# Kernel optimization log

Measured on AMD Instinct MI355X. Metric: run time of the kernel, lower is better.

Reference implementation:

```python
import jax, jax.numpy as jnp
import numpy as np

WAYS, SHOTS = 32, 64
N = WAYS * SHOTS
XDIM, CIN = 84, 3
FLAT = 10 * 19 * 19  # 3610 after conv/pool stack
ZDIM = 2 * 32 * 4    # 256

def _conv2d(x, w, b):
    y = jax.lax.conv_general_dilated(x, w, (1, 1), 'VALID',
        dimension_numbers=('NCHW', 'OIHW', 'NCHW'))
    return y + b[None, :, None, None]

def _maxpool2(x):
    return jax.lax.reduce_window(x, -jnp.inf, jax.lax.max,
        (1, 1, 2, 2), (1, 1, 2, 2), 'VALID')

def setup_inputs() -> dict:
    key = jax.random.key(0)
    ks = jax.random.split(key, 32)
    rn = lambda k, shape, s=0.05: jax.random.normal(k, shape, jnp.float32) * s
    labels = jax.random.randint(ks[0], (N,), 0, WAYS)
    y = jax.nn.one_hot(labels, WAYS, dtype=jnp.float32)
    z = lambda n: jnp.zeros((n,), jnp.float32)
    return {
        'x': jax.random.normal(ks[1], (N, CIN, XDIM, XDIM), jnp.float32),
        'y': y,
        'conv1_w': rn(ks[2], (10, CIN, 3, 3)), 'conv1_b': z(10),
        'conv2_w': rn(ks[3], (10, 10, 3, 3)), 'conv2_b': z(10),
        'enc_w': rn(ks[4], (FLAT, 64)), 'enc_b': z(64),
        't1_w': rn(ks[5], (3, 4), 0.2), 't1_b': z(4),
        'te2_w1': rn(ks[6], (256, 128)), 'te2_b1': z(128),
        'te2_w2': rn(ks[7], (128, 32)), 'te2_b2': z(32),
        't2_w': rn(ks[8], (3, 4), 0.2), 't2_b': z(4),
        'om_mu_w': rn(ks[9], (256, 1)), 'om_mu_b': z(1),
        'om_sd_w': rn(ks[10], (256, 1)), 'om_sd_b': z(1),
        'ga_w': rn(ks[11], (128, 64)), 'ga_b': z(64),
        'ga_mu_w': rn(ks[12], (64, 5)), 'ga_mu_b': z(5),
        'ga_sd_w': rn(ks[13], (64, 5)), 'ga_sd_b': z(5),
        'ze_w': rn(ks[14], (128, 64)), 'ze_b': z(64),
        'ze_mu_w': rn(ks[15], (64, ZDIM)), 'ze_mu_b': z(ZDIM),
        'ze_sd_w': rn(ks[16], (64, ZDIM)), 'ze_sd_b': z(ZDIM),
        'do_sample': 0,
    }

def _kl_std_normal(mu, sigma):
    # KL(N(mu, sigma) || N(0, 1)), summed
    return jnp.sum(-jnp.log(sigma) + 0.5 * (sigma * sigma + mu * mu) - 0.5)

def _forward(x, y, conv1_w, conv1_b, conv2_w, conv2_b, enc_w, enc_b,
             t1_w, t1_b, te2_w1, te2_b1, te2_w2, te2_b2, t2_w, t2_b,
             om_mu_w, om_mu_b, om_sd_w, om_sd_b,
             ga_w, ga_b, ga_mu_w, ga_mu_b, ga_sd_w, ga_sd_b,
             ze_w, ze_b, ze_mu_w, ze_mu_b, ze_sd_w, ze_sd_b):
    relu = jax.nn.relu
    # class encoder: conv-relu-pool x2 + flatten + linear -> [N, 64]
    h = _maxpool2(relu(_conv2d(x, conv1_w, conv1_b)))
    h = _maxpool2(relu(_conv2d(h, conv2_w, conv2_b)))
    h = h.reshape(h.shape[0], -1) @ enc_w + enc_b  # [N, 64]
    # statistics_pooling_1: per-class masked var/mean/cardinality (vectorized over classes)
    y_sum = jnp.sum(y, axis=1)           # [N]
    y_arg = jnp.argmax(y, axis=1)        # [N]
    cls_mask = ((y_arg[None, :] == jnp.arange(WAYS)[:, None]) &
                (y_sum[None, :] > 0)).astype(jnp.float32)  # [W, N]
    xm = h[None, :, :] * cls_mask[:, :, None]              # [W, N, 64]
    mean = jnp.mean(xm, axis=1)                            # [W, 64]
    var = jnp.var(xm, axis=1, ddof=1)                      # unbiased, matches torch.var_mean
    card = (jnp.sum(y[None, :, :] * cls_mask[:, :, None], axis=(1, 2)) - 1.0) / (SHOTS - 1.0)  # [W]
    cs = jnp.stack([mean, var, jnp.broadcast_to(card[:, None], (WAYS, 64))], axis=2)  # [W, 64, 3]
    cs = relu(cs @ t1_w + t1_b).reshape(WAYS, -1)          # [W, 256]
    # statistics_pooling_2
    ts = relu(cs @ te2_w1 + te2_b1) @ te2_w2 + te2_b2      # [W, 32]
    t = jnp.stack([jnp.mean(ts, axis=0), jnp.var(ts, axis=0, ddof=1),
                   jnp.broadcast_to(jnp.sum(card), (32,))], axis=1)  # [32, 3]
    t = relu(t @ t2_w + t2_b).reshape(1, -1)               # [1, 128]
    # omega (use_s=True: heads applied to class_summary directly)
    mu_o = relu(cs @ om_mu_w + om_mu_b)[:, 0]              # [W]
    sd_o = jax.nn.softplus(relu(cs @ om_sd_w + om_sd_b)[:, 0])
    # gamma
    eg = relu(t @ ga_w + ga_b)                             # [1, 64]
    mu_g = relu(eg @ ga_mu_w + ga_mu_b)[0]                 # [5]
    sd_g = jax.nn.softplus(relu(eg @ ga_sd_w + ga_sd_b)[0])
    # zeta
    ez = relu(t @ ze_w + ze_b)                             # [1, 64]
    mu_z = relu(ez @ ze_mu_w + ze_mu_b)[0]                 # [256]
    sd_z = jax.nn.softplus(relu(ez @ ze_sd_w + ze_sd_b)[0])
    kl = _kl_std_normal(mu_o, sd_o) + _kl_std_normal(mu_g, sd_g) + _kl_std_normal(mu_z, sd_z)
    # deterministic path (do_sample=False -> distribution means); concat for a single output
    return jnp.concatenate([mu_o, mu_g, mu_z, kl[None]])   # [W + 5 + 256 + 1]

def reference(x, y, conv1_w, conv1_b, conv2_w, conv2_b, enc_w, enc_b,
              t1_w, t1_b, te2_w1, te2_b1, te2_w2, te2_b2, t2_w, t2_b,
              om_mu_w, om_mu_b, om_sd_w, om_sd_b,
              ga_w, ga_b, ga_mu_w, ga_mu_b, ga_sd_w, ga_sd_b,
              ze_w, ze_b, ze_mu_w, ze_mu_b, ze_sd_w, ze_sd_b, do_sample):
    return _forward(x, y, conv1_w, conv1_b, conv2_w, conv2_b, enc_w, enc_b,
                    t1_w, t1_b, te2_w1, te2_b1, te2_w2, te2_b2, t2_w, t2_b,
                    om_mu_w, om_mu_b, om_sd_w, om_sd_b,
                    ga_w, ga_b, ga_mu_w, ga_mu_b, ga_sd_w, ga_sd_b,
                    ze_w, ze_b, ze_mu_w, ze_mu_b, ze_sd_w, ze_sd_b)
```

## Files before the change

kernel.cpp:

```cpp
#include <hip/hip_runtime.h>
#include <math.h>

#define WAYS 32
#define NTOT 2048
#define XD 84
#define FLAT 3610
#define KSPLIT 16
#define KCHUNK 226

__device__ __forceinline__ float softplus_f(float x) {
    return (x > 20.f) ? x : log1pf(expf(x));
}
__device__ __forceinline__ float kl_f(float mu, float sd) {
    return -logf(sd) + 0.5f * (sd * sd + mu * mu) - 0.5f;
}

struct Out10 { float v[10]; };

__global__ __launch_bounds__(256, 4) void k_conv(
        const float* __restrict__ x,
        const float* __restrict__ w1, const float* __restrict__ b1,
        const float* __restrict__ w2, const float* __restrict__ b2,
        float* __restrict__ p2) {
    __shared__ __align__(16) float u_s[3 * 22 * 84];
    __shared__ __align__(16) float w1t[27 * 12];
    __shared__ __align__(16) float w2t[90 * 16];

    const int tid  = threadIdx.x;
    const int img  = blockIdx.x & 2047;
    const int band = blockIdx.x >> 11;
    const int r0   = band * 4;
    const int nr   = (band < 4) ? 4 : 3;
    const int nq   = 2 * nr + 2;
    const int xr0  = 16 * band;
    const int nxr  = 2 * nq + 2;

    {
        const float* xg = x + (size_t)img * (3 * XD * XD);
        const int nv = (nxr * 84) >> 2;
        #pragma unroll
        for (int c = 0; c < 3; c++) {
            const float4* src = (const float4*)(xg + c * (XD * XD) + xr0 * 84);
            float4* dst = (float4*)(u_s + c * (22 * 84));
            for (int i = tid; i < nv; i += 256) dst[i] = src[i];
        }
    }
    for (int i = tid; i < 270; i += 256) {
        int oc = i / 27, r = i - oc * 27;
        w1t[r * 12 + oc] = w1[i];
    }
    for (int i = tid; i < 900; i += 256) {
        int oc = i / 90, r = i - oc * 90;
        int h = oc / 5, o = oc - h * 5;
        w2t[r * 16 + h * 8 + o] = w2[i];
    }
    float b1r[10];
    #pragma unroll
    for (int o = 0; o < 10; o++) b1r[o] = b1[o];
    __syncthreads();

    const int n1 = nq * 40;

    auto conv1_item = [&](int q, int p) -> Out10 {
        float acc[10][4];
        #pragma unroll
        for (int o = 0; o < 10; o++)
            #pragma unroll
            for (int j = 0; j < 4; j++) acc[o][j] = 0.f;
        #pragma unroll 1
        for (int c = 0; c < 3; c++) {
            float xp[4][4];
            #pragma unroll
            for (int rr = 0; rr < 4; rr++) {
                const float2* row =
                    (const float2*)&u_s[c * (22 * 84) + (2 * q + rr) * 84 + 2 * p];
                float2 lo = row[0], hi = row[1];
                xp[rr][0] = lo.x; xp[rr][1] = lo.y;
                xp[rr][2] = hi.x; xp[rr][3] = hi.y;
            }
            #pragma unroll
            for (int ky = 0; ky < 3; ky++) {
                #pragma unroll
                for (int kx = 0; kx < 3; kx++) {
                    const float* wr = &w1t[(c * 9 + ky * 3 + kx) * 12];
                    float4 wA = *(const float4*)(wr);
                    float4 wB = *(const float4*)(wr + 4);
                    float2 wC = *(const float2*)(wr + 8);
                    float wv[10] = {wA.x, wA.y, wA.z, wA.w,
                                    wB.x, wB.y, wB.z, wB.w,
                                    wC.x, wC.y};
                    #pragma unroll
                    for (int o = 0; o < 10; o++) {
                        float w = wv[o];
                        acc[o][0] = fmaf(xp[ky][kx],         w, acc[o][0]);
                        acc[o][1] = fmaf(xp[ky][kx + 1],     w, acc[o][1]);
                        acc[o][2] = fmaf(xp[ky + 1][kx],     w, acc[o][2]);
                        acc[o][3] = fmaf(xp[ky + 1][kx + 1], w, acc[o][3]);
                    }
                }
            }
        }
        Out10 r;
        #pragma unroll
        for (int o = 0; o < 10; o++) {
            float m = fmaxf(fmaxf(acc[o][0], acc[o][1]), fmaxf(acc[o][2], acc[o][3]));
            r.v[o] = fmaxf(m + b1r[o], 0.f);
        }
        return r;
    };

    Out10 A, B;
    {
        int q = tid / 40, p = tid - q * 40;
        A = conv1_item(q, p);
    }
    asm volatile("" ::: "memory");
    const int itB = tid + 256;
    const bool hasB = (itB < n1);
    if (hasB) {
        int q = itB / 40, p = itB - q * 40;
        B = conv1_item(q, p);
    }
    __syncthreads();

    {
        #pragma unroll
        for (int o = 0; o < 10; o++) u_s[o * 400 + tid] = A.v[o];
        if (hasB) {
            #pragma unroll
            for (int o = 0; o < 10; o++) u_s[o * 400 + itB] = B.v[o];
        }
    }
    __syncthreads();

    {
        const int npos = nr * 19;
        if (tid < 152) {
            int half = (tid >= 76) ? 1 : 0;
            int pos  = tid - 76 * half;
            if (pos < npos) {
                int pr = pos / 19;
                int pc = pos - pr * 19;
                float acc[5][4];
                #pragma unroll
                for (int o = 0; o < 5; o++)
                    #pragma unroll
                    for (int j = 0; j < 4; j++) acc[o][j] = 0.f;
                #pragma unroll 1
                for (int ic = 0; ic < 10; ic++) {
                    float xp[4][4];
                    #pragma unroll
                    for (int rr = 0; rr < 4; rr++) {
                        const float2* row =
                            (const float2*)&u_s[ic * 400 + (2 * pr + rr) * 40 + 2 * pc];
                        float2 lo = row[0], hi = row[1];
                        xp[rr][0] = lo.x; xp[rr][1] = lo.y;
                        xp[rr][2] = hi.x; xp[rr][3] = hi.y;
                    }
                    #pragma unroll
                    for (int ky = 0; ky < 3; ky++) {
                        #pragma unroll
                        for (int kx = 0; kx < 3; kx++) {
                            const float* wr = &w2t[(ic * 9 + ky * 3 + kx) * 16 + half * 8];
                            float4 wA = *(const float4*)(wr);
                            float w4 = wr[4];
                            float wv[5] = {wA.x, wA.y, wA.z, wA.w, w4};
                            #pragma unroll
                            for (int o = 0; o < 5; o++) {
                                float w = wv[o];
                                acc[o][0] = fmaf(xp[ky][kx],         w, acc[o][0]);
                                acc[o][1] = fmaf(xp[ky][kx + 1],     w, acc[o][1]);
                                acc[o][2] = fmaf(xp[ky + 1][kx],     w, acc[o][2]);
                                acc[o][3] = fmaf(xp[ky + 1][kx + 1], w, acc[o][3]);
                            }
                        }
                    }
                }
                float* outp = p2 + (size_t)img * FLAT;
                #pragma unroll
                for (int o = 0; o < 5; o++) {
                    int oc = half * 5 + o;
                    float m = fmaxf(fmaxf(acc[o][0], acc[o][1]), fmaxf(acc[o][2], acc[o][3]));
                    outp[oc * 361 + (r0 + pr) * 19 + pc] = fmaxf(m + b2[oc], 0.f);
                }
            }
        }
    }
}

__global__ void k_label(const float* __restrict__ y, int* __restrict__ label) {
    int n = blockIdx.x * 256 + threadIdx.x;
    if (n >= NTOT) return;
    const float* yr = y + n * WAYS;
    float best = yr[0]; int bi = 0;
    for (int k = 1; k < WAYS; k++) {
        float v = yr[k];
        if (v > best) { best = v; bi = k; }
    }
    label[n] = bi;
}

__global__ __launch_bounds__(256, 2) void k_enc(
        const float* __restrict__ A, const float* __restrict__ W,
        float* __restrict__ H) {
    __shared__ float a_s[32 * 66];
    __shared__ float w_s[32 * 64];
    int mb = blockIdx.x >> 4;
    int ks = blockIdx.x & 15;
    int row0 = mb * 64;
    int kbeg = ks * KCHUNK;
    int kend = min(kbeg + KCHUNK, FLAT);
    int tid = threadIdx.x;
    int tr = tid & 15, tc = tid >> 4;
    float acc[4][4] = {};

    for (int k0 = kbeg; k0 < kend; k0 += 32) {
        {
            int kk = tid & 31;
            int r  = tid >> 5;
            int gk = k0 + kk;
            #pragma unroll
            for (int i = 0; i < 8; i++) {
                int rr = r + i * 8;
                float v = (gk < kend) ? A[(size_t)(row0 + rr) * FLAT + gk] : 0.f;
                a_s[kk * 66 + rr] = v;
            }
            int c  = tid & 63;
            int kw = tid >> 6;
            #pragma unroll
            for (int i = 0; i < 8; i++) {
                int kk2 = kw + i * 4;
                int gk2 = k0 + kk2;
                float v = (gk2 < kend) ? W[(size_t)gk2 * 64 + c] : 0.f;
                w_s[kk2 * 64 + c] = v;
            }
        }
        __syncthreads();
        #pragma unroll 8
        for (int k = 0; k < 32; k++) {
            float av[4], wv[4];
            #pragma unroll
            for (int i = 0; i < 4; i++) av[i] = a_s[k * 66 + tr * 4 + i];
            #pragma unroll
            for (int j = 0; j < 4; j++) wv[j] = w_s[k * 64 + tc * 4 + j];
            #pragma unroll
            for (int i = 0; i < 4; i++)
                #pragma unroll
                for (int j = 0; j < 4; j++)
                    acc[i][j] = fmaf(av[i], wv[j], acc[i][j]);
        }
        __syncthreads();
    }
    #pragma unroll
    for (int i = 0; i < 4; i++)
        #pragma unroll
        for (int j = 0; j < 4; j++)
            atomicAdd(&H[(size_t)(row0 + tr * 4 + i) * 64 + tc * 4 + j], acc[i][j]);
}

__global__ __launch_bounds__(1024) void k_stats(
        const float* __restrict__ H, const float* __restrict__ encb,
        const int* __restrict__ label,
        const float* __restrict__ t1w, const float* __restrict__ t1b,
        float* __restrict__ cs, float* __restrict__ card) {
    __shared__ int   lbl_s[NTOT];
    __shared__ float rs[16][64], rs2[16][64];
    __shared__ int rc[16];
    int w = blockIdx.x;
    int tid = threadIdx.x;
    for (int i = tid; i < NTOT; i += 1024) lbl_s[i] = label[i];
    __syncthreads();
    int c = tid & 63, g = tid >> 6;
    float eb = encb[c];
    float s = 0.f, s2 = 0.f; int cnt = 0;
    #pragma unroll 4
    for (int n = g; n < NTOT; n += 16) {
        bool m = (lbl_s[n] == w);
        float hv = H[n * 64 + c] + eb;
        float hm = m ? hv : 0.f;
        s += hm; s2 += hm * hm; cnt += m ? 1 : 0;
    }
    rs[g][c] = s; rs2[g][c] = s2;
    if (c == 0) rc[g] = cnt;
    __syncthreads();
    if (g == 0) {
        float S = 0.f, S2 = 0.f; int CNT = 0;
        #pragma unroll
        for (int gg = 0; gg < 16; gg++) {
            S += rs[gg][c]; S2 += rs2[gg][c]; CNT += rc[gg];
        }
        float mean = S / 2048.f;
        float var  = (S2 - S * S / 2048.f) / 2047.f;
        float cd   = ((float)CNT - 1.f) / 63.f;
        #pragma unroll
        for (int j = 0; j < 4; j++)
            cs[w * 256 + c * 4 + j] =
                fmaxf(mean * t1w[j] + var * t1w[4 + j] + cd * t1w[8 + j] + t1b[j], 0.f);
        if (c == 0) card[w] = cd;
    }
}

__global__ __launch_bounds__(256) void k_head(
        const float* __restrict__ cs_g, const float* __restrict__ card,
        const float* __restrict__ te2w1, const float* __restrict__ te2b1,
        const float* __restrict__ te2w2, const float* __restrict__ te2b2,
        const float* __restrict__ t2w, const float* __restrict__ t2b,
        const float* __restrict__ omw, const float* __restrict__ omb,
        const float* __restrict__ osw, const float* __restrict__ osb,
        const float* __restrict__ gaw, const float* __restrict__ gab,
        const float* __restrict__ gmw, const float* __restrict__ gmb,
        const float* __restrict__ gsw, const float* __restrict__ gsb,
        const float* __restrict__ zew, const float* __restrict__ zeb,
        const float* __restrict__ zmw, const float* __restrict__ zmb,
        const float* __restrict__ zsw, const float* __restrict__ zsb,
        float* __restrict__ out) {
    __shared__ __align__(16) float cst[256 * 36];
    __shared__ __align__(16) float a1t[128 * 36];
    __shared__ float ts[32 * 32];
    __shared__ float tv[128];
    __shared__ float eg_s[64], ez_s[64];
    __shared__ float red[256];
    __shared__ float redb[512];
    int tid = threadIdx.x;

    for (int i = tid; i < 32 * 256; i += 256) {
        int w = i >> 8, k = i & 255;
        cst[k * 36 + w] = cs_g[i];
    }
    __syncthreads();

    {
        int wg = tid >> 5, jg = tid & 31;
        int w0 = wg * 4, j0 = jg * 4;
        float acc[4][4] = {};
        for (int k = 0; k < 256; k++) {
            float4 cv4 = *(const float4*)&cst[k * 36 + w0];
            float4 wv4 = *(const float4*)&te2w1[k * 128 + j0];
            float cva[4] = {cv4.x, cv4.y, cv4.z, cv4.w};
            float wva[4] = {wv4.x, wv4.y, wv4.z, wv4.w};
            #pragma unroll
            for (int i = 0; i < 4; i++)
                #pragma unroll
                for (int j = 0; j < 4; j++)
                    acc[i][j] = fmaf(cva[i], wva[j], acc[i][j]);
        }
        #pragma unroll
        for (int jj = 0; jj < 4; jj++) {
            float b = te2b1[j0 + jj];
            #pragma unroll
            for (int i = 0; i < 4; i++)
                a1t[(j0 + jj) * 36 + w0 + i] = fmaxf(acc[i][jj] + b, 0.f);
        }
    }
    __syncthreads();

    {
        int wg = tid >> 4, jg = tid & 15;
        int w0 = wg * 2, j0 = jg * 2;
        float acc[2][2] = {};
        for (int k = 0; k < 128; k++) {
            float2 a2 = *(const float2*)&a1t[k * 36 + w0];
            float2 b2v = *(const float2*)&te2w2[k * 32 + j0];
            acc[0][0] = fmaf(a2.x, b2v.x, acc[0][0]);
            acc[0][1] = fmaf(a2.x, b2v.y, acc[0][1]);
            acc[1][0] = fmaf(a2.y, b2v.x, acc[1][0]);
            acc[1][1] = fmaf(a2.y, b2v.y, acc[1][1]);
        }
        #pragma unroll
        for (int i = 0; i < 2; i++)
            #pragma unroll
            for (int j = 0; j < 2; j++)
                ts[(w0 + i) * 32 + (j0 + j)] = acc[i][j] + te2b2[j0 + j];
    }

    {
        int w = tid & 31, part = tid >> 5;
        int k0 = part * 32;
        float am = 0.f, as = 0.f;
        #pragma unroll 4
        for (int k = k0; k < k0 + 32; k++) {
            float cv = cst[k * 36 + w];
            am = fmaf(cv, omw[k], am);
            as = fmaf(cv, osw[k], as);
        }
        redb[part * 32 + w] = am;
        redb[256 + part * 32 + w] = as;
    }
    __syncthreads();

    float muo = 0.f, sdo = 1.f;
    if (tid < 32) {
        float am = 0.f, as = 0.f;
        #pragma unroll
        for (int p = 0; p < 8; p++) {
            am += redb[p * 32 + tid];
            as += redb[256 + p * 32 + tid];
        }
        muo = fmaxf(am + omb[0], 0.f);
        sdo = softplus_f(fmaxf(as + osb[0], 0.f));
        out[tid] = muo;
    } else if (tid < 64) {
        int t_ = tid - 32;
        float csum = 0.f;
        for (int w2 = 0; w2 < 32; w2++) csum += card[w2];
        float s = 0.f, s2 = 0.f;
        for (int w2 = 0; w2 < 32; w2++) { float v = ts[w2 * 32 + t_]; s += v; s2 += v * v; }
        float m  = s / 32.f;
        float vv = (s2 - s * s / 32.f) / 31.f;
        #pragma unroll
        for (int j = 0; j < 4; j++)
            tv[t_ * 4 + j] = fmaxf(m * t2w[j] + vv * t2w[4 + j] + csum * t2w[8 + j] + t2b[j], 0.f);
    }
    __syncthreads();

    {
        int j = tid & 63, part = tid >> 6;
        int k0 = part * 32;
        float ag = 0.f, az = 0.f;
        #pragma unroll 4
        for (int k = k0; k < k0 + 32; k++) {
            float t = tv[k];
            ag = fmaf(t, gaw[k * 64 + j], ag);
            az = fmaf(t, zew[k * 64 + j], az);
        }
        redb[part * 64 + j] = ag;
        redb[256 + part * 64 + j] = az;
    }
    __syncthreads();
    if (tid < 64) {
        float ag = gab[tid], az = zeb[tid];
        #pragma unroll
        for (int p = 0; p < 4; p++) {
            ag += redb[p * 64 + tid];
            az += redb[256 + p * 64 + tid];
        }
        eg_s[tid] = fmaxf(ag, 0.f);
        ez_s[tid] = fmaxf(az, 0.f);
    }
    __syncthreads();

    float r = 0.f;
    {
        int j = tid;
        float am = zmb[j], as = zsb[j];
        for (int k = 0; k < 64; k++) {
            float e = ez_s[k];
            am = fmaf(e, zmw[k * 256 + j], am);
            as = fmaf(e, zsw[k * 256 + j], as);
        }
        float mu = fmaxf(am, 0.f);
        float sd = softplus_f(fmaxf(as, 0.f));
        out[37 + j] = mu;
        r += kl_f(mu, sd);
    }
    if (tid < 5) {
        float am = gmb[tid], as = gsb[tid];
        for (int k = 0; k < 64; k++) {
            float e = eg_s[k];
            am = fmaf(e, gmw[k * 5 + tid], am);
            as = fmaf(e, gsw[k * 5 + tid], as);
        }
        float mu = fmaxf(am, 0.f);
        float sd = softplus_f(fmaxf(as, 0.f));
        out[32 + tid] = mu;
        r += kl_f(mu, sd);
    }
    if (tid < 32) r += kl_f(muo, sdo);
    red[tid] = r;
    __syncthreads();
    for (int s = 128; s > 0; s >>= 1) {
        if (tid < s) red[tid] += red[tid + s];
        __syncthreads();
    }
    if (tid == 0) out[293] = red[0];
}

extern "C" void kernel_launch(void* const* d_in, const int* in_sizes, int n_in,
                              void* d_out, int out_size, void* d_ws, size_t ws_size,
                              hipStream_t stream) {
    const float* x    = (const float*)d_in[0];
    const float* y    = (const float*)d_in[1];
    const float* w1   = (const float*)d_in[2];
    const float* b1   = (const float*)d_in[3];
    const float* w2   = (const float*)d_in[4];
    const float* b2   = (const float*)d_in[5];
    const float* encw = (const float*)d_in[6];
    const float* encb = (const float*)d_in[7];
    const float* t1w  = (const float*)d_in[8];
    const float* t1b  = (const float*)d_in[9];
    const float* te2w1 = (const float*)d_in[10];
    const float* te2b1 = (const float*)d_in[11];
    const float* te2w2 = (const float*)d_in[12];
    const float* te2b2 = (const float*)d_in[13];
    const float* t2w  = (const float*)d_in[14];
    const float* t2b  = (const float*)d_in[15];
    const float* omw  = (const float*)d_in[16];
    const float* omb  = (const float*)d_in[17];
    const float* osw  = (const float*)d_in[18];
    const float* osb  = (const float*)d_in[19];
    const float* gaw  = (const float*)d_in[20];
    const float* gab  = (const float*)d_in[21];
    const float* gmw  = (const float*)d_in[22];
    const float* gmb  = (const float*)d_in[23];
    const float* gsw  = (const float*)d_in[24];
    const float* gsb  = (const float*)d_in[25];
    const float* zew  = (const float*)d_in[26];
    const float* zeb  = (const float*)d_in[27];
    const float* zmw  = (const float*)d_in[28];
    const float* zmb  = (const float*)d_in[29];
    const float* zsw  = (const float*)d_in[30];
    const float* zsb  = (const float*)d_in[31];
    float* out = (float*)d_out;

    float* p2   = (float*)d_ws;
    float* H    = p2 + (size_t)NTOT * FLAT;
    int*   lbl  = (int*)(H + NTOT * 64);
    float* cs   = (float*)(lbl + NTOT);
    float* card = cs + 32 * 256;

    hipMemsetAsync(H, 0, NTOT * 64 * sizeof(float), stream);
    hipLaunchKernelGGL(k_conv, dim3(NTOT * 5), dim3(256), 0, stream, x, w1, b1, w2, b2, p2);
    hipLaunchKernelGGL(k_label, dim3(8), dim3(256), 0, stream, y, lbl);
    hipLaunchKernelGGL(k_enc, dim3(32 * KSPLIT), dim3(256), 0, stream, p2, encw, H);
    hipLaunchKernelGGL(k_stats, dim3(32), dim3(1024), 0, stream, H, encb, lbl, t1w, t1b, cs, card);
    hipLaunchKernelGGL(k_head, dim3(1), dim3(256), 0, stream, cs, card,
                       te2w1, te2b1, te2w2, te2b2, t2w, t2b,
                       omw, omb, osw, osb, gaw, gab, gmw, gmb, gsw, gsb,
                       zew, zeb, zmw, zmb, zsw, zsb, out);
}
```

Measured before the change: 641.8 us.

## Halve conv band height for more blocks and vectorize encoder shared loads

The fused conv kernel now processes 2 pooled output rows per block instead of 4, doubling the grid, so each thread computes a single conv1 item and shared memory per block shrinks. This aims to improve occupancy and load balance, at the cost of recomputing more overlapping conv1 rows and reloading more input halo rows. The encoder GEMM pads its A tile to 68 columns and uses float4 shared loads to cut LDS instruction count.

```diff
diff --git a/kernel.cpp b/kernel.cpp
--- a/kernel.cpp
+++ b/kernel.cpp
@@ -15,24 +15,23 @@
     return -logf(sd) + 0.5f * (sd * sd + mu * mu) - 0.5f;
 }
 
-struct Out10 { float v[10]; };
-
-__global__ __launch_bounds__(256, 4) void k_conv(
+__global__ __launch_bounds__(256, 5) void k_conv(
         const float* __restrict__ x,
         const float* __restrict__ w1, const float* __restrict__ b1,
         const float* __restrict__ w2, const float* __restrict__ b2,
         float* __restrict__ p2) {
-    __shared__ __align__(16) float u_s[3 * 22 * 84];
+    __shared__ __align__(16) float xs[3 * 14 * 84];
+    __shared__ __align__(16) float p1s[10 * 6 * 40];
     __shared__ __align__(16) float w1t[27 * 12];
     __shared__ __align__(16) float w2t[90 * 16];
 
     const int tid  = threadIdx.x;
     const int img  = blockIdx.x & 2047;
     const int band = blockIdx.x >> 11;
-    const int r0   = band * 4;
-    const int nr   = (band < 4) ? 4 : 3;
+    const int r0   = band * 2;
+    const int nr   = (band < 9) ? 2 : 1;
     const int nq   = 2 * nr + 2;
-    const int xr0  = 16 * band;
+    const int xr0  = 8 * band;
     const int nxr  = 2 * nq + 2;
 
     {
@@ -41,7 +40,7 @@
         #pragma unroll
         for (int c = 0; c < 3; c++) {
             const float4* src = (const float4*)(xg + c * (XD * XD) + xr0 * 84);
-            float4* dst = (float4*)(u_s + c * (22 * 84));
+            float4* dst = (float4*)(xs + c * (14 * 84));
             for (int i = tid; i < nv; i += 256) dst[i] = src[i];
         }
     }
@@ -59,130 +58,106 @@
     for (int o = 0; o < 10; o++) b1r[o] = b1[o];
     __syncthreads();
 
-    const int n1 = nq * 40;
-
-    auto conv1_item = [&](int q, int p) -> Out10 {
-        float acc[10][4];
-        #pragma unroll
-        for (int o = 0; o < 10; o++)
-            #pragma unroll
-            for (int j = 0; j < 4; j++) acc[o][j] = 0.f;
-        #pragma unroll 1
-        for (int c = 0; c < 3; c++) {
-            float xp[4][4];
-            #pragma unroll
-            for (int rr = 0; rr < 4; rr++) {
-                const float2* row =
-                    (const float2*)&u_s[c * (22 * 84) + (2 * q + rr) * 84 + 2 * p];
-                float2 lo = row[0], hi = row[1];
-                xp[rr][0] = lo.x; xp[rr][1] = lo.y;
-                xp[rr][2] = hi.x; xp[rr][3] = hi.y;
-            }
-            #pragma unroll
-            for (int ky = 0; ky < 3; ky++) {
-                #pragma unroll
-                for (int kx = 0; kx < 3; kx++) {
-                    const float* wr = &w1t[(c * 9 + ky * 3 + kx) * 12];
-                    float4 wA = *(const float4*)(wr);
-                    float4 wB = *(const float4*)(wr + 4);
-                    float2 wC = *(const float2*)(wr + 8);
-                    float wv[10] = {wA.x, wA.y, wA.z, wA.w,
-                                    wB.x, wB.y, wB.z, wB.w,
-                                    wC.x, wC.y};
+    {
+        const int n1 = nq * 40;
+        if (tid < n1) {
+            int q = tid / 40;
+            int p = tid - q * 40;
+            float acc[10][4];
+            #pragma unroll
+            for (int o = 0; o < 10; o++)
+                #pragma unroll
+                for (int j = 0; j < 4; j++) acc[o][j] = 0.f;
+            #pragma unroll 1
+            for (int c = 0; c < 3; c++) {
+                float xp[4][4];
+                #pragma unroll
+                for (int rr = 0; rr < 4; rr++) {
+                    const float2* row =
+                        (const float2*)&xs[c * (14 * 84) + (2 * q + rr) * 84 + 2 * p];
+                    float2 lo = row[0], hi = row[1];
+                    xp[rr][0] = lo.x; xp[rr][1] = lo.y;
+                    xp[rr][2] = hi.x; xp[rr][3] = hi.y;
+                }
+                #pragma unroll
+                for (int ky = 0; ky < 3; ky++) {
                     #pragma unroll
-                    for (int o = 0; o < 10; o++) {
-                        float w = wv[o];
-                        acc[o][0] = fmaf(xp[ky][kx],         w, acc[o][0]);
-                        acc[o][1] = fmaf(xp[ky][kx + 1],     w, acc[o][1]);
-                        acc[o][2] = fmaf(xp[ky + 1][kx],     w, acc[o][2]);
-                        acc[o][3] = fmaf(xp[ky + 1][kx + 1], w, acc[o][3]);
+                    for (int kx = 0; kx < 3; kx++) {
+                        const float* wr = &w1t[(c * 9 + ky * 3 + kx) * 12];
+                        float4 wA = *(const float4*)(wr);
+                        float4 wB = *(const float4*)(wr + 4);
+                        float2 wC = *(const float2*)(wr + 8);
+                        float wv[10] = {wA.x, wA.y, wA.z, wA.w,
+                                        wB.x, wB.y, wB.z, wB.w,
+                                        wC.x, wC.y};
+                        #pragma unroll
+                        for (int o = 0; o < 10; o++) {
+                            float w = wv[o];
+                            acc[o][0] = fmaf(xp[ky][kx],         w, acc[o][0]);
+                            acc[o][1] = fmaf(xp[ky][kx + 1],     w, acc[o][1]);
+                            acc[o][2] = fmaf(xp[ky + 1][kx],     w, acc[o][2]);
+                            acc[o][3] = fmaf(xp[ky + 1][kx + 1], w, acc[o][3]);
+                        }
                     }
                 }
             }
-        }
-        Out10 r;
-        #pragma unroll
-        for (int o = 0; o < 10; o++) {
-            float m = fmaxf(fmaxf(acc[o][0], acc[o][1]), fmaxf(acc[o][2], acc[o][3]));
-            r.v[o] = fmaxf(m + b1r[o], 0.f);
-        }
-        return r;
-    };
-
-    Out10 A, B;
-    {
-        int q = tid / 40, p = tid - q * 40;
-        A = conv1_item(q, p);
-    }
-    asm volatile("" ::: "memory");
-    const int itB = tid + 256;
-    const bool hasB = (itB < n1);
-    if (hasB) {
-        int q = itB / 40, p = itB - q * 40;
-        B = conv1_item(q, p);
-    }
-    __syncthreads();
-
-    {
-        #pragma unroll
-        for (int o = 0; o < 10; o++) u_s[o * 400 + tid] = A.v[o];
-        if (hasB) {
-            #pragma unroll
-            for (int o = 0; o < 10; o++) u_s[o * 400 + itB] = B.v[o];
+            #pragma unroll
+            for (int o = 0; o < 10; o++) {
+                float m = fmaxf(fmaxf(acc[o][0], acc[o][1]), fmaxf(acc[o][2], acc[o][3]));
+                p1s[o * 240 + q * 40 + p] = fmaxf(m + b1r[o], 0.f);
+            }
         }
     }
     __syncthreads();
 
     {
         const int npos = nr * 19;
-        if (tid < 152) {
-            int half = (tid >= 76) ? 1 : 0;
-            int pos  = tid - 76 * half;
-            if (pos < npos) {
-                int pr = pos / 19;
-                int pc = pos - pr * 19;
-                float acc[5][4];
-                #pragma unroll
-                for (int o = 0; o < 5; o++)
+        if (tid < 2 * npos) {
+            int half = (tid >= npos) ? 1 : 0;
+            int pos  = tid - npos * half;
+            int pr = pos / 19;
+            int pc = pos - pr * 19;
+            float acc[5][4];
+            #pragma unroll
+            for (int o = 0; o < 5; o++)
+                #pragma unroll
+                for (int j = 0; j < 4; j++) acc[o][j] = 0.f;
+            #pragma unroll 1
+            for (int ic = 0; ic < 10; ic++) {
+                float xp[4][4];
+                #pragma unroll
+                for (int rr = 0; rr < 4; rr++) {
+                    const float2* row =
+                        (const float2*)&p1s[ic * 240 + (2 * pr + rr) * 40 + 2 * pc];
+                    float2 lo = row[0], hi = row[1];
+                    xp[rr][0] = lo.x; xp[rr][1] = lo.y;
+                    xp[rr][2] = hi.x; xp[rr][3] = hi.y;
+                }
+                #pragma unroll
+                for (int ky = 0; ky < 3; ky++) {
                     #pragma unroll
-                    for (int j = 0; j < 4; j++) acc[o][j] = 0.f;
-                #pragma unroll 1
-                for (int ic = 0; ic < 10; ic++) {
-                    float xp[4][4];
-                    #pragma unroll
-                    for (int rr = 0; rr < 4; rr++) {
-                        const float2* row =
-                            (const float2*)&u_s[ic * 400 + (2 * pr + rr) * 40 + 2 * pc];
-                        float2 lo = row[0], hi = row[1];
-                        xp[rr][0] = lo.x; xp[rr][1] = lo.y;
-                        xp[rr][2] = hi.x; xp[rr][3] = hi.y;
-                    }
-                    #pragma unroll
-                    for (int ky = 0; ky < 3; ky++) {
+                    for (int kx = 0; kx < 3; kx++) {
+                        const float* wr = &w2t[(ic * 9 + ky * 3 + kx) * 16 + half * 8];
+                        float4 wA = *(const float4*)(wr);
+                        float w4 = wr[4];
+                        float wv[5] = {wA.x, wA.y, wA.z, wA.w, w4};
                         #pragma unroll
-                        for (int kx = 0; kx < 3; kx++) {
-                            const float* wr = &w2t[(ic * 9 + ky * 3 + kx) * 16 + half * 8];
-                            float4 wA = *(const float4*)(wr);
-                            float w4 = wr[4];
-                            float wv[5] = {wA.x, wA.y, wA.z, wA.w, w4};
-                            #pragma unroll
-                            for (int o = 0; o < 5; o++) {
-                                float w = wv[o];
-                                acc[o][0] = fmaf(xp[ky][kx],         w, acc[o][0]);
-                                acc[o][1] = fmaf(xp[ky][kx + 1],     w, acc[o][1]);
-                                acc[o][2] = fmaf(xp[ky + 1][kx],     w, acc[o][2]);
-                                acc[o][3] = fmaf(xp[ky + 1][kx + 1], w, acc[o][3]);
-                            }
+                        for (int o = 0; o < 5; o++) {
+                            float w = wv[o];
+                            acc[o][0] = fmaf(xp[ky][kx],         w, acc[o][0]);
+                            acc[o][1] = fmaf(xp[ky][kx + 1],     w, acc[o][1]);
+                            acc[o][2] = fmaf(xp[ky + 1][kx],     w, acc[o][2]);
+                            acc[o][3] = fmaf(xp[ky + 1][kx + 1], w, acc[o][3]);
                         }
                     }
                 }
-                float* outp = p2 + (size_t)img * FLAT;
-                #pragma unroll
-                for (int o = 0; o < 5; o++) {
-                    int oc = half * 5 + o;
-                    float m = fmaxf(fmaxf(acc[o][0], acc[o][1]), fmaxf(acc[o][2], acc[o][3]));
-                    outp[oc * 361 + (r0 + pr) * 19 + pc] = fmaxf(m + b2[oc], 0.f);
-                }
+            }
+            float* outp = p2 + (size_t)img * FLAT;
+            #pragma unroll
+            for (int o = 0; o < 5; o++) {
+                int oc = half * 5 + o;
+                float m = fmaxf(fmaxf(acc[o][0], acc[o][1]), fmaxf(acc[o][2], acc[o][3]));
+                outp[oc * 361 + (r0 + pr) * 19 + pc] = fmaxf(m + b2[oc], 0.f);
             }
         }
     }
@@ -203,8 +178,8 @@
 __global__ __launch_bounds__(256, 2) void k_enc(
         const float* __restrict__ A, const float* __restrict__ W,
         float* __restrict__ H) {
-    __shared__ float a_s[32 * 66];
-    __shared__ float w_s[32 * 64];
+    __shared__ __align__(16) float a_s[32 * 68];
+    __shared__ __align__(16) float w_s[32 * 64];
     int mb = blockIdx.x >> 4;
     int ks = blockIdx.x & 15;
     int row0 = mb * 64;
@@ -223,7 +198,7 @@
             for (int i = 0; i < 8; i++) {
                 int rr = r + i * 8;
                 float v = (gk < kend) ? A[(size_t)(row0 + rr) * FLAT + gk] : 0.f;
-                a_s[kk * 66 + rr] = v;
+                a_s[kk * 68 + rr] = v;
             }
             int c  = tid & 63;
             int kw = tid >> 6;
@@ -238,11 +213,10 @@
         __syncthreads();
         #pragma unroll 8
         for (int k = 0; k < 32; k++) {
-            float av[4], wv[4];
-            #pragma unroll
-            for (int i = 0; i < 4; i++) av[i] = a_s[k * 66 + tr * 4 + i];
-            #pragma unroll
-            for (int j = 0; j < 4; j++) wv[j] = w_s[k * 64 + tc * 4 + j];
+            float4 av4 = *(const float4*)&a_s[k * 68 + tr * 4];
+            float4 wv4 = *(const float4*)&w_s[k * 64 + tc * 4];
+            float av[4] = {av4.x, av4.y, av4.z, av4.w};
+            float wv[4] = {wv4.x, wv4.y, wv4.z, wv4.w};
             #pragma unroll
             for (int i = 0; i < 4; i++)
                 #pragma unroll
@@ -519,7 +493,7 @@
     float* card = cs + 32 * 256;
 
     hipMemsetAsync(H, 0, NTOT * 64 * sizeof(float), stream);
-    hipLaunchKernelGGL(k_conv, dim3(NTOT * 5), dim3(256), 0, stream, x, w1, b1, w2, b2, p2);
+    hipLaunchKernelGGL(k_conv, dim3(NTOT * 10), dim3(256), 0, stream, x, w1, b1, w2, b2, p2);
     hipLaunchKernelGGL(k_label, dim3(8), dim3(256), 0, stream, y, lbl);
     hipLaunchKernelGGL(k_enc, dim3(32 * KSPLIT), dim3(256), 0, stream, p2, encw, H);
     hipLaunchKernelGGL(k_stats, dim3(32), dim3(1024), 0, stream, H, encb, lbl, t1w, t1b, cs, card);
```

New measurement: 667.3 us. 4.0% more time.
